# Performance work log

Hardware: AMD Instinct MI355X
Metric: run time of the kernel (lower is better)

Reference implementation:

```python
import jax, jax.numpy as jnp
import numpy as np

NEG_SLOPE = 0.2

def setup_inputs() -> dict:
    key = jax.random.key(0)
    k1, k2, k3, k4 = jax.random.split(key, 4)
    N, K, C_IN, C_OUT = 8192, 4, 512, 512
    inputs = jax.random.normal(k1, (N, C_IN), dtype=jnp.float32)
    adj_set = jax.random.uniform(k2, (K, N, N), dtype=jnp.float32)
    att = jax.random.uniform(k3, (K,), dtype=jnp.float32)
    # xavier_uniform for w
    limit = float(np.sqrt(6.0 / (C_IN + C_OUT)))
    w = jax.random.uniform(k4, (C_IN, C_OUT), minval=-limit, maxval=limit, dtype=jnp.float32)
    b = jnp.zeros((C_OUT,), dtype=jnp.float32)
    return {"inputs": inputs, "adj_set": adj_set, "att": att, "w": w, "b": b}

def reference(inputs, adj_set, att, w, b):
    # support: [N, C_out]
    support = inputs @ w + b
    # residual=True path: outputs = sum_i att[i] * (adj_i @ support)
    #                             = (sum_i att[i] * adj_i) @ support
    combined_adj = jnp.einsum('k,knm->nm', att, adj_set)  # [N, N]
    outputs = combined_adj @ support                       # [N, C_out]
    # LeakyReLU(negative_slope=0.2)
    return jnp.where(outputs >= 0, outputs, NEG_SLOPE * outputs)
```

## Files before the change

### kernel.cpp

```cpp
#include <hip/hip_runtime.h>

#define LP 40

typedef __attribute__((ext_vector_type(8))) short short8;
typedef __attribute__((ext_vector_type(4))) short short4t;
typedef __attribute__((ext_vector_type(4))) float f32x4;

__device__ __forceinline__ short f2bf(float f) {
  unsigned u = __builtin_bit_cast(unsigned, f);
  u += 0x7FFFu + ((u >> 16) & 1u);
  return (short)(u >> 16);
}

__device__ __forceinline__ float lrelu(float v) { return v >= 0.f ? v : 0.2f * v; }

__global__ __launch_bounds__(256) void k_wt(const float* __restrict__ w,
                                            short* __restrict__ wt) {
  __shared__ float t[64][65];
  int c0 = (blockIdx.x & 7) * 64;
  int n0 = (blockIdx.x >> 3) * 64;
  int r  = threadIdx.x >> 4;
  int q4 = (threadIdx.x & 15) * 4;
  for (int i = 0; i < 4; i++) {
    int c = r + i * 16;
    f32x4 v = *(const f32x4*)(w + (size_t)(c0 + c) * 512 + (n0 + q4));
    t[c][q4 + 0] = v[0]; t[c][q4 + 1] = v[1]; t[c][q4 + 2] = v[2]; t[c][q4 + 3] = v[3];
  }
  __syncthreads();
  for (int i = 0; i < 4; i++) {
    int n = r + i * 16;
    short4t o;
    for (int j = 0; j < 4; j++) o[j] = f2bf(t[q4 + j][n]);
    *(short4t*)(wt + (size_t)(n0 + n) * 512 + (c0 + q4)) = o;
  }
}

__global__ __launch_bounds__(512, 2) void k_support(const float* __restrict__ inp,
                                                    const short* __restrict__ wt,
                                                    const float* __restrict__ bias,
                                                    short* __restrict__ sup) {
  __shared__ __align__(16) short As[512 * LP];
  __shared__ __align__(16) short Bs[64 * LP];
  const int tid = threadIdx.x;
  const int m0 = blockIdx.x * 64;
  const int wave = tid >> 6, lane = tid & 63;
  const int wn = wave >> 1, wm = wave & 1;
  const int lr = lane & 15, lk = lane >> 4;
  const int bm = tid >> 3, bk = (tid & 7) * 4;
  f32x4 acc[8][2] = {};
  short8 ar[4]; f32x4 br;
  auto loadA = [&](int s) {
    const short* p = wt + (size_t)tid * 512 + s * 32;
    ar[0] = *(const short8*)(p);      ar[1] = *(const short8*)(p + 8);
    ar[2] = *(const short8*)(p + 16); ar[3] = *(const short8*)(p + 24);
  };
  auto loadB = [&](int s) {
    br = *(const f32x4*)(inp + (size_t)(m0 + bm) * 512 + s * 32 + bk);
  };
  loadA(0); loadB(0);
  for (int s = 0; s < 16; s++) {
    short* ad = As + tid * LP;
    *(short8*)(ad) = ar[0]; *(short8*)(ad + 8) = ar[1];
    *(short8*)(ad + 16) = ar[2]; *(short8*)(ad + 24) = ar[3];
    short4t bo;
    for (int j = 0; j < 4; j++) bo[j] = f2bf(br[j]);
    *(short4t*)(Bs + bm * LP + bk) = bo;
    __syncthreads();
    if (s + 1 < 16) { loadA(s + 1); loadB(s + 1); }
    short8 af[8], bfr[2];
    for (int nf = 0; nf < 8; nf++)
      af[nf] = *(const short8*)(As + (wn * 128 + nf * 16 + lr) * LP + lk * 8);
    for (int mf = 0; mf < 2; mf++)
      bfr[mf] = *(const short8*)(Bs + (wm * 32 + mf * 16 + lr) * LP + lk * 8);
    for (int nf = 0; nf < 8; nf++)
      for (int mf = 0; mf < 2; mf++)
        acc[nf][mf] = __builtin_amdgcn_mfma_f32_16x16x32_bf16(af[nf], bfr[mf], acc[nf][mf], 0, 0, 0);
    __syncthreads();
  }
  for (int nf = 0; nf < 8; nf++) {
    int nb = wn * 128 + nf * 16 + lk * 4;
    for (int mf = 0; mf < 2; mf++) {
      int m = m0 + wm * 32 + mf * 16 + lr;
      for (int j = 0; j < 4; j++) {
        int n = nb + j;
        sup[(size_t)n * 8192 + m] = f2bf(acc[nf][mf][j] + bias[n]);
      }
    }
  }
}

__global__ __launch_bounds__(512, 2) void k_main(const float* __restrict__ adj,
                                                 const float* __restrict__ att,
                                                 const short* __restrict__ sup,
                                                 float* __restrict__ part,
                                                 float* __restrict__ outp,
                                                 int ksplit) {
  __shared__ __align__(16) short Bs[2][128 * LP];
  const int tid = threadIdx.x;
  const int b = blockIdx.x;
  const int xpk = 8 / ksplit;
  const int xcd = b & 7;
  const int kc = xcd / xpk;
  const int m0 = ((b >> 3) * xpk + (xcd % xpk)) * 128;
  const int kchunk = 8192 / ksplit;
  const int nsteps = kchunk / 32;
  const int kbase = kc * kchunk;
  const float t0 = att[0], t1 = att[1], t2 = att[2], t3 = att[3];
  const int wave = tid >> 6, lane = tid & 63;
  const int lr = lane & 15, lk = lane >> 4;
  const int srow = tid >> 2, koff = (tid & 3) * 8;
  f32x4 acc[4][8] = {};
  const float* adjp = adj + (size_t)(m0 + srow) * 8192 + kbase + koff;
  const short* supp = sup + (size_t)(wave * 64 + lr) * 8192 + kbase + lk * 8;
  f32x4 br[8];
  auto loadAdj = [&](int s) {
    const float* q = adjp + (size_t)s * 32;
#pragma unroll
    for (int mt = 0; mt < 4; mt++) {
      br[mt * 2]     = __builtin_nontemporal_load((const f32x4*)(q + ((size_t)mt << 26)));
      br[mt * 2 + 1] = __builtin_nontemporal_load((const f32x4*)(q + ((size_t)mt << 26) + 4));
    }
  };
  loadAdj(0);
  int p = 0;
  for (int s = 0; s < nsteps; s++) {
    short8 af[4];
#pragma unroll
    for (int nf = 0; nf < 4; nf++)
      af[nf] = *(const short8*)(supp + (size_t)(nf * 16) * 8192 + s * 32);
    short8 bo;
#pragma unroll
    for (int k2 = 0; k2 < 8; k2++) {
      int h = k2 >> 2, j = k2 & 3;
      float c = t0 * br[h][j] + t1 * br[2 + h][j] + t2 * br[4 + h][j] + t3 * br[6 + h][j];
      bo[k2] = f2bf(c);
    }
    *(short8*)(Bs[p] + srow * LP + koff) = bo;
    __syncthreads();
    if (s + 1 < nsteps) loadAdj(s + 1);
    short8 bfr[8];
#pragma unroll
    for (int mf = 0; mf < 8; mf++)
      bfr[mf] = *(const short8*)(Bs[p] + (mf * 16 + lr) * LP + lk * 8);
#pragma unroll
    for (int nf = 0; nf < 4; nf++)
#pragma unroll
      for (int mf = 0; mf < 8; mf++)
        acc[nf][mf] = __builtin_amdgcn_mfma_f32_16x16x32_bf16(af[nf], bfr[mf], acc[nf][mf], 0, 0, 0);
    p ^= 1;
  }
#pragma unroll
  for (int nf = 0; nf < 4; nf++) {
    int n = wave * 64 + nf * 16 + lk * 4;
#pragma unroll
    for (int mf = 0; mf < 8; mf++) {
      int m = m0 + mf * 16 + lr;
      f32x4 v = acc[nf][mf];
      if (ksplit == 1) {
        for (int j = 0; j < 4; j++) v[j] = lrelu(v[j]);
        __builtin_nontemporal_store(v, (f32x4*)(outp + (size_t)m * 512 + n));
      } else {
        __builtin_nontemporal_store(v, (f32x4*)(part + ((size_t)kc << 22) + (size_t)m * 512 + n));
      }
    }
  }
}

__global__ __launch_bounds__(256) void k_reduce(const float* __restrict__ part,
                                                float* __restrict__ outp, int ksplit) {
  const size_t total = (size_t)8192 * 512 / 4;
  for (size_t i = (size_t)blockIdx.x * 256 + threadIdx.x; i < total;
       i += (size_t)gridDim.x * 256) {
    f32x4 a = __builtin_nontemporal_load((const f32x4*)(part + i * 4));
    for (int k = 1; k < ksplit; k++) {
      f32x4 bv = __builtin_nontemporal_load((const f32x4*)(part + ((size_t)k << 22) + i * 4));
      for (int j = 0; j < 4; j++) a[j] += bv[j];
    }
    f32x4 v;
    for (int j = 0; j < 4; j++) v[j] = lrelu(a[j]);
    __builtin_nontemporal_store(v, (f32x4*)(outp + i * 4));
  }
}

extern "C" void kernel_launch(void* const* d_in, const int* in_sizes, int n_in,
                              void* d_out, int out_size, void* d_ws, size_t ws_size,
                              hipStream_t stream) {
  const float* inputs = (const float*)d_in[0];
  const float* adj    = (const float*)d_in[1];
  const float* att    = (const float*)d_in[2];
  const float* w      = (const float*)d_in[3];
  const float* bias   = (const float*)d_in[4];
  float* outp = (float*)d_out;

  char* ws = (char*)d_ws;
  short* sup  = (short*)(ws);
  short* wt   = (short*)(ws + (8u << 20));
  float* part = (float*)(ws + (9u << 20));

  const size_t base = (9ull << 20), psz = (1ull << 24);
  int ksplit = 1;
  if (ws_size >= base + 4 * psz) ksplit = 4;
  else if (ws_size >= base + 2 * psz) ksplit = 2;

  k_wt<<<64, 256, 0, stream>>>(w, wt);
  k_support<<<128, 512, 0, stream>>>(inputs, wt, bias, sup);
  k_main<<<64 * ksplit, 512, 0, stream>>>(adj, att, sup, part, outp, ksplit);
  if (ksplit > 1) k_reduce<<<1024, 256, 0, stream>>>(part, outp, ksplit);
}
```

Before: 337.3 us.

## Drop LDS staging in main GEMM, load adj fragments directly into registers

The main kernel no longer stages the combined adjacency tile through shared memory. Each wave now loads its own 16-row adjacency fragment straight from global memory, combines the four matrices in registers, and feeds MFMA directly, covering 256 output columns per wave. The M tile shrinks to 64 rows, ksplit is fixed at 2 and made a template parameter, and the barriers are removed. In exchange, the support operand is read redundantly by more blocks, there is no software prefetch of the adjacency loads, and register pressure rises.

Result: slower. 839.4 us (+148.9%).

```diff
diff --git a/kernel.cpp b/kernel.cpp
--- a/kernel.cpp
+++ b/kernel.cpp
@@ -89,79 +89,67 @@
   }
 }
 
+template <int KSPLIT>
 __global__ __launch_bounds__(512, 2) void k_main(const float* __restrict__ adj,
                                                  const float* __restrict__ att,
                                                  const short* __restrict__ sup,
                                                  float* __restrict__ part,
-                                                 float* __restrict__ outp,
-                                                 int ksplit) {
-  __shared__ __align__(16) short Bs[2][128 * LP];
+                                                 float* __restrict__ outp) {
+  constexpr int KCH = 8192 / KSPLIT;
+  constexpr int NSTEPS = KCH / 32;
   const int tid = threadIdx.x;
   const int b = blockIdx.x;
-  const int xpk = 8 / ksplit;
+  const int xpk = 8 / KSPLIT;
   const int xcd = b & 7;
   const int kc = xcd / xpk;
-  const int m0 = ((b >> 3) * xpk + (xcd % xpk)) * 128;
-  const int kchunk = 8192 / ksplit;
-  const int nsteps = kchunk / 32;
-  const int kbase = kc * kchunk;
+  const int m0 = ((b >> 3) * xpk + (xcd % xpk)) * 64;
+  const int kbase = kc * KCH;
   const float t0 = att[0], t1 = att[1], t2 = att[2], t3 = att[3];
-  const int wave = tid >> 6, lane = tid & 63;
+  const int w = tid >> 6, lane = tid & 63;
   const int lr = lane & 15, lk = lane >> 4;
-  const int srow = tid >> 2, koff = (tid & 3) * 8;
-  f32x4 acc[4][8] = {};
-  const float* adjp = adj + (size_t)(m0 + srow) * 8192 + kbase + koff;
-  const short* supp = sup + (size_t)(wave * 64 + lr) * 8192 + kbase + lk * 8;
-  f32x4 br[8];
-  auto loadAdj = [&](int s) {
-    const float* q = adjp + (size_t)s * 32;
+  const int nw = w & 1, mw = w >> 1;
+  const float* ab = adj + (size_t)(m0 + mw * 16 + lr) * 8192 + kbase + lk * 8;
+  const short* sb = sup + (size_t)(nw * 256 + lr) * 8192 + kbase + lk * 8;
+  f32x4 acc[16] = {};
+
+  for (int s = 0; s < NSTEPS; s++) {
+    const float* p = ab + s * 32;
+    f32x4 b0a = __builtin_nontemporal_load((const f32x4*)(p));
+    f32x4 b0b = __builtin_nontemporal_load((const f32x4*)(p + 4));
+    f32x4 b1a = __builtin_nontemporal_load((const f32x4*)(p + (1ull << 26)));
+    f32x4 b1b = __builtin_nontemporal_load((const f32x4*)(p + (1ull << 26) + 4));
+    f32x4 b2a = __builtin_nontemporal_load((const f32x4*)(p + (2ull << 26)));
+    f32x4 b2b = __builtin_nontemporal_load((const f32x4*)(p + (2ull << 26) + 4));
+    f32x4 b3a = __builtin_nontemporal_load((const f32x4*)(p + (3ull << 26)));
+    f32x4 b3b = __builtin_nontemporal_load((const f32x4*)(p + (3ull << 26) + 4));
+    short8 af[16];
 #pragma unroll
-    for (int mt = 0; mt < 4; mt++) {
-      br[mt * 2]     = __builtin_nontemporal_load((const f32x4*)(q + ((size_t)mt << 26)));
-      br[mt * 2 + 1] = __builtin_nontemporal_load((const f32x4*)(q + ((size_t)mt << 26) + 4));
+    for (int nf = 0; nf < 16; nf++)
+      af[nf] = *(const short8*)(sb + (size_t)(nf * 16) * 8192 + s * 32);
+    f32x4 cA, cB;
+#pragma unroll
+    for (int e = 0; e < 4; e++) {
+      cA[e] = t0 * b0a[e] + t1 * b1a[e] + t2 * b2a[e] + t3 * b3a[e];
+      cB[e] = t0 * b0b[e] + t1 * b1b[e] + t2 * b2b[e] + t3 * b3b[e];
     }
-  };
-  loadAdj(0);
-  int p = 0;
-  for (int s = 0; s < nsteps; s++) {
-    short8 af[4];
+    short8 bfr;
 #pragma unroll
-    for (int nf = 0; nf < 4; nf++)
-      af[nf] = *(const short8*)(supp + (size_t)(nf * 16) * 8192 + s * 32);
-    short8 bo;
+    for (int e = 0; e < 4; e++) { bfr[e] = f2bf(cA[e]); bfr[4 + e] = f2bf(cB[e]); }
 #pragma unroll
-    for (int k2 = 0; k2 < 8; k2++) {
-      int h = k2 >> 2, j = k2 & 3;
-      float c = t0 * br[h][j] + t1 * br[2 + h][j] + t2 * br[4 + h][j] + t3 * br[6 + h][j];
-      bo[k2] = f2bf(c);
-    }
-    *(short8*)(Bs[p] + srow * LP + koff) = bo;
-    __syncthreads();
-    if (s + 1 < nsteps) loadAdj(s + 1);
-    short8 bfr[8];
+    for (int nf = 0; nf < 16; nf++)
+      acc[nf] = __builtin_amdgcn_mfma_f32_16x16x32_bf16(af[nf], bfr, acc[nf], 0, 0, 0);
+  }
+
 #pragma unroll
-    for (int mf = 0; mf < 8; mf++)
-      bfr[mf] = *(const short8*)(Bs[p] + (mf * 16 + lr) * LP + lk * 8);
-#pragma unroll
-    for (int nf = 0; nf < 4; nf++)
-#pragma unroll
-      for (int mf = 0; mf < 8; mf++)
-        acc[nf][mf] = __builtin_amdgcn_mfma_f32_16x16x32_bf16(af[nf], bfr[mf], acc[nf][mf], 0, 0, 0);
-    p ^= 1;
-  }
-#pragma unroll
-  for (int nf = 0; nf < 4; nf++) {
-    int n = wave * 64 + nf * 16 + lk * 4;
-#pragma unroll
-    for (int mf = 0; mf < 8; mf++) {
-      int m = m0 + mf * 16 + lr;
-      f32x4 v = acc[nf][mf];
-      if (ksplit == 1) {
-        for (int j = 0; j < 4; j++) v[j] = lrelu(v[j]);
-        __builtin_nontemporal_store(v, (f32x4*)(outp + (size_t)m * 512 + n));
-      } else {
-        __builtin_nontemporal_store(v, (f32x4*)(part + ((size_t)kc << 22) + (size_t)m * 512 + n));
-      }
+  for (int nf = 0; nf < 16; nf++) {
+    int n = nw * 256 + nf * 16 + lk * 4;
+    int m = m0 + mw * 16 + lr;
+    f32x4 v = acc[nf];
+    if (KSPLIT == 1) {
+      for (int j = 0; j < 4; j++) v[j] = lrelu(v[j]);
+      __builtin_nontemporal_store(v, (f32x4*)(outp + (size_t)m * 512 + n));
+    } else {
+      __builtin_nontemporal_store(v, (f32x4*)(part + ((size_t)kc << 22) + (size_t)m * 512 + n));
     }
   }
 }
@@ -198,12 +186,14 @@
   float* part = (float*)(ws + (9u << 20));
 
   const size_t base = (9ull << 20), psz = (1ull << 24);
-  int ksplit = 1;
-  if (ws_size >= base + 4 * psz) ksplit = 4;
-  else if (ws_size >= base + 2 * psz) ksplit = 2;
 
   k_wt<<<64, 256, 0, stream>>>(w, wt);
   k_support<<<128, 512, 0, stream>>>(inputs, wt, bias, sup);
-  k_main<<<64 * ksplit, 512, 0, stream>>>(adj, att, sup, part, outp, ksplit);
-  if (ksplit > 1) k_reduce<<<1024, 256, 0, stream>>>(part, outp, ksplit);
+
+  if (ws_size >= base + 2 * psz) {
+    k_main<2><<<256, 512, 0, stream>>>(adj, att, sup, part, outp);
+    k_reduce<<<1024, 256, 0, stream>>>(part, outp, 2);
+  } else {
+    k_main<1><<<128, 512, 0, stream>>>(adj, att, sup, part, outp);
+  }
 }
```
